# Kernel optimization log

Measured on AMD Instinct MI355X. Metric: run time of the kernel, lower is better.

## Reference

```python
import jax, jax.numpy as jnp
import numpy as np

VOCAB, T, E, H, O, B = 401, 140, 128, 256, 3, 4096


def setup_inputs() -> dict:
    key = jax.random.key(0)
    ks = jax.random.split(key, 8)
    s_e = 1.0 / np.sqrt(H)
    return {
        "input": jax.random.randint(ks[0], (B, T), 0, VOCAB),
        "hidden": jnp.zeros((B, H), dtype=jnp.float32),
        "embed": jax.random.normal(ks[1], (VOCAB, E), dtype=jnp.float32),
        "W_ih": jax.random.uniform(ks[2], (3 * H, E), jnp.float32, -s_e, s_e),
        "W_hh": jax.random.uniform(ks[3], (3 * H, H), jnp.float32, -s_e, s_e),
        "b_ih": jax.random.uniform(ks[4], (3 * H,), jnp.float32, -s_e, s_e),
        "b_hh": jax.random.uniform(ks[5], (3 * H,), jnp.float32, -s_e, s_e),
        "W_out": jax.random.uniform(ks[6], (O, H), jnp.float32, -s_e, s_e),
        "b_out": jax.random.uniform(ks[7], (O,), jnp.float32, -s_e, s_e),
    }


def reference(input, hidden, embed, W_ih, W_hh, b_ih, b_hh, W_out, b_out):
    # Embedding lookup: [B, T, E]
    x = embed[input]
    # Precompute input-side gate projections for all timesteps: [B, T, 3H]
    gi = jnp.einsum("bte,ge->btg", x, W_ih) + b_ih

    def step(h, gi_t):
        gh = h @ W_hh.T + b_hh  # [B, 3H]
        i_r, i_z, i_n = jnp.split(gi_t, 3, axis=-1)
        h_r, h_z, h_n = jnp.split(gh, 3, axis=-1)
        r = jax.nn.sigmoid(i_r + h_r)
        z = jax.nn.sigmoid(i_z + h_z)
        n = jnp.tanh(i_n + r * h_n)
        h_new = (1.0 - z) * n + z * h
        return h_new, None

    h_final, _ = jax.lax.scan(step, hidden, jnp.swapaxes(gi, 0, 1))
    logits = h_final @ W_out.T + b_out  # [B, O]
    return jax.nn.log_softmax(logits, axis=1), h_final
```

## Files before the change

### kernel.cpp

```cpp
#include <hip/hip_runtime.h>

typedef __attribute__((ext_vector_type(8))) short short8;
typedef __attribute__((ext_vector_type(4))) float f32x4;
typedef unsigned short ushort_t;
typedef unsigned int uint_t;

#define VOCAB 401
#define T_ 140
#define E_ 128
#define H_ 256
#define B_ 4096
#define HPAD 264

__device__ float Gf[VOCAB * 768];
__device__ ushort_t WhhB[768 * H_];

__device__ __forceinline__ float bf2f(ushort_t u) {
  union { uint_t i; float f; } x; x.i = ((uint_t)u) << 16; return x.f;
}
__device__ __forceinline__ ushort_t f2bf(float f) {
  union { float f; uint_t i; } x; x.f = f;
  uint_t r = x.i + 0x7FFFu + ((x.i >> 16) & 1u);
  return (ushort_t)(r >> 16);
}
__device__ __forceinline__ float fast_sigmoid(float x) {
  return __builtin_amdgcn_rcpf(1.f + __builtin_amdgcn_exp2f(-1.442695041f * x));
}
__device__ __forceinline__ float fast_tanh(float x) {
  return 1.f - 2.f * __builtin_amdgcn_rcpf(1.f + __builtin_amdgcn_exp2f(2.885390082f * x));
}
__device__ __forceinline__ float ldf(const void* p, size_t i, int isb) {
  return isb ? bf2f(((const ushort_t*)p)[i]) : ((const float*)p)[i];
}
__device__ __forceinline__ void ld8f(const void* p, size_t idx, int isb, float* o) {
  if (isb) {
    short8 v = *(const short8*)((const ushort_t*)p + idx);
#pragma unroll
    for (int e = 0; e < 8; ++e) o[e] = bf2f((ushort_t)v[e]);
  } else {
    f32x4 a = *(const f32x4*)((const float*)p + idx);
    f32x4 b = *(const f32x4*)((const float*)p + idx + 4);
#pragma unroll
    for (int e = 0; e < 4; ++e) { o[e] = a[e]; o[4 + e] = b[e]; }
  }
}
__device__ __forceinline__ int block_probe_isbf16(const ushort_t* embed_raw, int* s) {
  if (threadIdx.x < 64) {
    ushort_t v = embed_raw[2 * threadIdx.x];
    int e = (v >> 7) & 0xFF;
    unsigned long long m = __ballot(e >= 100 && e <= 140);
    if (threadIdx.x == 0) *s = (__popcll(m) >= 40) ? 1 : 0;
  }
  __syncthreads();
  return *s;
}

__global__ void prep(const void* __restrict__ W_hh,
                     const void* __restrict__ embed,
                     const void* __restrict__ W_ih,
                     const void* __restrict__ b_ih,
                     const void* __restrict__ b_hh) {
  __shared__ float emb[8][E_];
  __shared__ int sISB;
  const int isb = block_probe_isbf16((const ushort_t*)embed, &sISB);
  const int bid = blockIdx.x;
  const int j = threadIdx.x;

  if (bid >= 153) {
    int i4 = ((bid - 153) * 256 + j) * 4;
    if (isb) {
      *(uint2*)&WhhB[i4] = *(const uint2*)((const ushort_t*)W_hh + i4);
    } else {
      f32x4 v = *(const f32x4*)((const float*)W_hh + i4);
      uint2 pk;
      pk.x = (uint_t)f2bf(v[0]) | ((uint_t)f2bf(v[1]) << 16);
      pk.y = (uint_t)f2bf(v[2]) | ((uint_t)f2bf(v[3]) << 16);
      *(uint2*)&WhhB[i4] = pk;
    }
    return;
  }

  const int vb = bid / 3;
  const int g  = bid - vb * 3;
  for (int idx = j; idx < 8 * E_; idx += 256) {
    int s = idx >> 7, e = idx & 127;
    int v = vb * 8 + s; if (v > VOCAB - 1) v = VOCAB - 1;
    emb[s][e] = ldf(embed, (size_t)v * E_ + e, isb);
  }
  __syncthreads();
  const int row = g * H_ + j;
  float acc[8];
#pragma unroll
  for (int s = 0; s < 8; ++s) acc[s] = 0.f;
  for (int k8 = 0; k8 < E_ / 8; ++k8) {
    float wv[8];
    ld8f(W_ih, (size_t)row * E_ + k8 * 8, isb, wv);
#pragma unroll
    for (int s = 0; s < 8; ++s)
#pragma unroll
      for (int e = 0; e < 8; ++e) acc[s] += emb[s][k8 * 8 + e] * wv[e];
  }
  float bias = ldf(b_ih, row, isb) + ((g < 2) ? ldf(b_hh, row, isb) : 0.f);
#pragma unroll
  for (int s = 0; s < 8; ++s) {
    int v = vb * 8 + s;
    if (v < VOCAB) Gf[v * 768 + row] = acc[s] + bias;
  }
}

__launch_bounds__(1024)
__global__ void gru_persist(const int* __restrict__ input,
                            const void* __restrict__ hidden,
                            const void* __restrict__ b_hh,
                            const void* __restrict__ W_out,
                            const void* __restrict__ b_out,
                            const ushort_t* __restrict__ embed_raw,
                            void* __restrict__ out) {
  __shared__ ushort_t hB[2][16 * HPAD];
  __shared__ float bhhn[H_];
  __shared__ int ids[16 * (T_ + 1)];
  __shared__ int sISB;

  const int isb  = block_probe_isbf16(embed_raw, &sISB);
  const int tid  = threadIdx.x;
  const int w    = tid >> 6;
  const int lane = tid & 63;
  const int quad = lane >> 4;
  const int col  = lane & 15;
  const int wg   = blockIdx.x;
  const int u0   = w << 4;
  const int u0q  = u0 + (quad << 2);

  if (tid < 512) {
    int r = tid >> 5, c0 = (tid & 31) << 3;
    size_t gi = (size_t)(wg * 16 + r) * H_ + c0;
    ushort_t* dst = &hB[0][r * HPAD + c0];
    if (isb) {
      *(short8*)dst = *(const short8*)((const ushort_t*)hidden + gi);
    } else {
      float tmp[8];
      ld8f(hidden, gi, 0, tmp);
#pragma unroll
      for (int e = 0; e < 8; ++e) dst[e] = f2bf(tmp[e]);
    }
  }
  if (tid < H_) bhhn[tid] = ldf(b_hh, 512 + tid, isb);
  for (int k = tid; k < 16 * (T_ + 1); k += 1024) {
    int b = k / (T_ + 1), t = k - b * (T_ + 1);
    ids[k] = (t < T_) ? input[(size_t)wg * 16 * T_ + b * T_ + t] * 3072 : 0;
  }

  short8 wA[3][8];
#pragma unroll
  for (int g = 0; g < 3; ++g) {
    const ushort_t* wrow = WhhB + (size_t)(g * H_ + u0 + col) * H_ + (quad << 3);
#pragma unroll
    for (int kt = 0; kt < 8; ++kt) wA[g][kt] = *(const short8*)(wrow + kt * 32);
  }

  __syncthreads();

  float hreg[4];
#pragma unroll
  for (int i = 0; i < 4; ++i)
    hreg[i] = bf2f(hB[0][col * HPAD + u0q + i]);

  const int idbase = col * (T_ + 1);
  const char* gB = (const char*)Gf + (size_t)u0q * 4;

  f32x4 accr, accz, gin;
  {
    int goff = ids[idbase];
    accr = *(const f32x4*)(gB + goff);
    accz = *(const f32x4*)(gB + goff + 1024);
    gin  = *(const f32x4*)(gB + goff + 2048);
  }

#pragma unroll 2
  for (int t = 0; t < T_; ++t) {
    const int cur = t & 1;
    const int nxt = cur ^ 1;
    const ushort_t* hr = &hB[cur][col * HPAD + (quad << 3)];
    const int goff_n = ids[idbase + t + 1];
    f32x4 bhv = *(const f32x4*)&bhhn[u0q];

#pragma unroll
    for (int kt = 0; kt < 8; ++kt) {
      short8 b = *(const short8*)(hr + kt * 32);
      accr = __builtin_amdgcn_mfma_f32_16x16x32_bf16(wA[0][kt], b, accr, 0, 0, 0);
      accz = __builtin_amdgcn_mfma_f32_16x16x32_bf16(wA[1][kt], b, accz, 0, 0, 0);
    }
    f32x4 an = bhv;
    float r_[4], z_[4];
#pragma unroll
    for (int kt = 0; kt < 8; ++kt) {
      short8 b = *(const short8*)(hr + kt * 32);
      an = __builtin_amdgcn_mfma_f32_16x16x32_bf16(wA[2][kt], b, an, 0, 0, 0);
      if (kt < 4) r_[kt] = fast_sigmoid(accr[kt]);
      else        z_[kt - 4] = fast_sigmoid(accz[kt - 4]);
    }

    uint_t rr[4];
#pragma unroll
    for (int i = 0; i < 4; ++i) {
      float n = fast_tanh(gin[i] + r_[i] * an[i]);
      float h = n + z_[i] * (hreg[i] - n);
      hreg[i] = h;
      union { float f; uint_t u; } c; c.f = h;
      rr[i] = c.u + 0x7FFFu + ((c.u >> 16) & 1u);
    }
    ushort_t* hw = &hB[nxt][col * HPAD + u0q];
    *(uint_t*)&hw[0] = __builtin_amdgcn_perm(rr[1], rr[0], 0x07060302);
    *(uint_t*)&hw[2] = __builtin_amdgcn_perm(rr[3], rr[2], 0x07060302);

    accr = *(const f32x4*)(gB + goff_n);
    accz = *(const f32x4*)(gB + goff_n + 1024);
    gin  = *(const f32x4*)(gB + goff_n + 2048);

    asm volatile("s_waitcnt lgkmcnt(0)\n\ts_barrier" ::: "memory");
  }

  {
    const ushort_t* hrow = &hB[0][w * HPAD + (lane << 2)];
    float h0 = bf2f(hrow[0]), h1 = bf2f(hrow[1]), h2 = bf2f(hrow[2]), h3 = bf2f(hrow[3]);
    float d[3];
#pragma unroll
    for (int o = 0; o < 3; ++o) {
      size_t base = (size_t)o * H_ + (lane << 2);
      d[o] = ldf(W_out, base, isb) * h0 + ldf(W_out, base + 1, isb) * h1 +
             ldf(W_out, base + 2, isb) * h2 + ldf(W_out, base + 3, isb) * h3;
      for (int off = 1; off < 64; off <<= 1) d[o] += __shfl_xor(d[o], off);
    }
    if (lane == 0) {
      float l0 = d[0] + ldf(b_out, 0, isb);
      float l1 = d[1] + ldf(b_out, 1, isb);
      float l2 = d[2] + ldf(b_out, 2, isb);
      float m = fmaxf(l0, fmaxf(l1, l2));
      float s = __builtin_amdgcn_exp2f((l0 - m) * 1.442695041f) +
                __builtin_amdgcn_exp2f((l1 - m) * 1.442695041f) +
                __builtin_amdgcn_exp2f((l2 - m) * 1.442695041f);
      float ls = __builtin_amdgcn_logf(s) * 0.6931471806f;
      size_t ob = (size_t)(wg * 16 + w) * 3;
      float o0 = l0 - m - ls, o1 = l1 - m - ls, o2 = l2 - m - ls;
      if (isb) {
        ushort_t* ob16 = (ushort_t*)out;
        ob16[ob] = f2bf(o0); ob16[ob + 1] = f2bf(o1); ob16[ob + 2] = f2bf(o2);
      } else {
        float* of = (float*)out;
        of[ob] = o0; of[ob + 1] = o1; of[ob + 2] = o2;
      }
    }
  }
  {
    int e = tid << 2;
    int bb = e >> 8, uu = e & 255;
    const ushort_t* src = &hB[0][bb * HPAD + uu];
    size_t oi = 12288 + (size_t)wg * 4096 + e;
    if (isb) {
      *(uint2*)((ushort_t*)out + oi) = *(const uint2*)src;
    } else {
      float* of = (float*)out;
      of[oi] = bf2f(src[0]); of[oi + 1] = bf2f(src[1]);
      of[oi + 2] = bf2f(src[2]); of[oi + 3] = bf2f(src[3]);
    }
  }
}

extern "C" void kernel_launch(void* const* d_in, const int* in_sizes, int n_in,
                              void* d_out, int out_size, void* d_ws, size_t ws_size,
                              hipStream_t stream) {
  (void)in_sizes; (void)n_in; (void)out_size; (void)d_ws; (void)ws_size;
  const int* input = (const int*)d_in[0];
  const void* hidden = d_in[1];
  const void* embed  = d_in[2];
  const void* W_ih   = d_in[3];
  const void* W_hh   = d_in[4];
  const void* b_ih   = d_in[5];
  const void* b_hh   = d_in[6];
  const void* W_out  = d_in[7];
  const void* b_out  = d_in[8];

  prep<<<345, 256, 0, stream>>>(W_hh, embed, W_ih, b_ih, b_hh);
  gru_persist<<<B_ / 16, 1024, 0, stream>>>(input, hidden, b_hh, W_out, b_out,
                                            (const ushort_t*)embed, d_out);
}
```

Before: 363.6 us.

## Fold activation exponent scales into weights and biases; restructure GRU step loop

Pre-scales W_hh rows, the input-gate table Gf and the n-gate hidden bias by the sigmoid and tanh exp2 constants during prep. This removes the per-element multiplies before exp2 in the recurrent loop. The loop is also manually unrolled by two with precomputed double-buffer pointers, the bias load is hoisted out of the loop, and the three gate MFMAs are interleaved in a single k-loop with the activations computed afterward. Scaling before the bf16 rounding of W_hh changes rounding slightly, and issuing all activations after the MFMAs gives up overlap of the r/z sigmoids with the n-gate MFMA chain.

```diff
diff --git a/kernel.cpp b/kernel.cpp
--- a/kernel.cpp
+++ b/kernel.cpp
@@ -12,6 +12,9 @@
 #define B_ 4096
 #define HPAD 264
 
+#define SIG_K -1.442695041f
+#define TANH_K 2.885390082f
+
 __device__ float Gf[VOCAB * 768];
 __device__ ushort_t WhhB[768 * H_];
 
@@ -22,12 +25,6 @@
   union { float f; uint_t i; } x; x.f = f;
   uint_t r = x.i + 0x7FFFu + ((x.i >> 16) & 1u);
   return (ushort_t)(r >> 16);
-}
-__device__ __forceinline__ float fast_sigmoid(float x) {
-  return __builtin_amdgcn_rcpf(1.f + __builtin_amdgcn_exp2f(-1.442695041f * x));
-}
-__device__ __forceinline__ float fast_tanh(float x) {
-  return 1.f - 2.f * __builtin_amdgcn_rcpf(1.f + __builtin_amdgcn_exp2f(2.885390082f * x));
 }
 __device__ __forceinline__ float ldf(const void* p, size_t i, int isb) {
   return isb ? bf2f(((const ushort_t*)p)[i]) : ((const float*)p)[i];
@@ -68,15 +65,21 @@
 
   if (bid >= 153) {
     int i4 = ((bid - 153) * 256 + j) * 4;
+    float sc = ((i4 >> 8) < 512) ? SIG_K : TANH_K;
+    float v[4];
     if (isb) {
-      *(uint2*)&WhhB[i4] = *(const uint2*)((const ushort_t*)W_hh + i4);
+      uint2 raw = *(const uint2*)((const ushort_t*)W_hh + i4);
+      v[0] = bf2f((ushort_t)(raw.x & 0xffff)); v[1] = bf2f((ushort_t)(raw.x >> 16));
+      v[2] = bf2f((ushort_t)(raw.y & 0xffff)); v[3] = bf2f((ushort_t)(raw.y >> 16));
     } else {
-      f32x4 v = *(const f32x4*)((const float*)W_hh + i4);
-      uint2 pk;
-      pk.x = (uint_t)f2bf(v[0]) | ((uint_t)f2bf(v[1]) << 16);
-      pk.y = (uint_t)f2bf(v[2]) | ((uint_t)f2bf(v[3]) << 16);
-      *(uint2*)&WhhB[i4] = pk;
-    }
+      f32x4 f = *(const f32x4*)((const float*)W_hh + i4);
+#pragma unroll
+      for (int e = 0; e < 4; ++e) v[e] = f[e];
+    }
+    uint2 pk;
+    pk.x = (uint_t)f2bf(v[0] * sc) | ((uint_t)f2bf(v[1] * sc) << 16);
+    pk.y = (uint_t)f2bf(v[2] * sc) | ((uint_t)f2bf(v[3] * sc) << 16);
+    *(uint2*)&WhhB[i4] = pk;
     return;
   }
 
@@ -89,6 +92,7 @@
   }
   __syncthreads();
   const int row = g * H_ + j;
+  const float sc = (g < 2) ? SIG_K : TANH_K;
   float acc[8];
 #pragma unroll
   for (int s = 0; s < 8; ++s) acc[s] = 0.f;
@@ -104,7 +108,7 @@
 #pragma unroll
   for (int s = 0; s < 8; ++s) {
     int v = vb * 8 + s;
-    if (v < VOCAB) Gf[v * 768 + row] = acc[s] + bias;
+    if (v < VOCAB) Gf[v * 768 + row] = (acc[s] + bias) * sc;
   }
 }
 
@@ -144,7 +148,7 @@
       for (int e = 0; e < 8; ++e) dst[e] = f2bf(tmp[e]);
     }
   }
-  if (tid < H_) bhhn[tid] = ldf(b_hh, 512 + tid, isb);
+  if (tid < H_) bhhn[tid] = TANH_K * ldf(b_hh, 512 + tid, isb);
   for (int k = tid; k < 16 * (T_ + 1); k += 1024) {
     int b = k / (T_ + 1), t = k - b * (T_ + 1);
     ids[k] = (t < T_) ? input[(size_t)wg * 16 * T_ + b * T_ + t] * 3072 : 0;
@@ -164,9 +168,15 @@
 #pragma unroll
   for (int i = 0; i < 4; ++i)
     hreg[i] = bf2f(hB[0][col * HPAD + u0q + i]);
+  const f32x4 bhv = *(const f32x4*)&bhhn[u0q];
 
   const int idbase = col * (T_ + 1);
   const char* gB = (const char*)Gf + (size_t)u0q * 4;
+
+  const ushort_t* hr0 = &hB[0][col * HPAD + (quad << 3)];
+  const ushort_t* hr1 = &hB[1][col * HPAD + (quad << 3)];
+  ushort_t* hw0 = &hB[1][col * HPAD + u0q];
+  ushort_t* hw1 = &hB[0][col * HPAD + u0q];
 
   f32x4 accr, accz, gin;
   {
@@ -176,49 +186,42 @@
     gin  = *(const f32x4*)(gB + goff + 2048);
   }
 
-#pragma unroll 2
-  for (int t = 0; t < T_; ++t) {
-    const int cur = t & 1;
-    const int nxt = cur ^ 1;
-    const ushort_t* hr = &hB[cur][col * HPAD + (quad << 3)];
-    const int goff_n = ids[idbase + t + 1];
-    f32x4 bhv = *(const f32x4*)&bhhn[u0q];
-
-#pragma unroll
-    for (int kt = 0; kt < 8; ++kt) {
-      short8 b = *(const short8*)(hr + kt * 32);
-      accr = __builtin_amdgcn_mfma_f32_16x16x32_bf16(wA[0][kt], b, accr, 0, 0, 0);
-      accz = __builtin_amdgcn_mfma_f32_16x16x32_bf16(wA[1][kt], b, accz, 0, 0, 0);
-    }
-    f32x4 an = bhv;
-    float r_[4], z_[4];
-#pragma unroll
-    for (int kt = 0; kt < 8; ++kt) {
-      short8 b = *(const short8*)(hr + kt * 32);
-      an = __builtin_amdgcn_mfma_f32_16x16x32_bf16(wA[2][kt], b, an, 0, 0, 0);
-      if (kt < 4) r_[kt] = fast_sigmoid(accr[kt]);
-      else        z_[kt - 4] = fast_sigmoid(accz[kt - 4]);
-    }
-
-    uint_t rr[4];
-#pragma unroll
-    for (int i = 0; i < 4; ++i) {
-      float n = fast_tanh(gin[i] + r_[i] * an[i]);
-      float h = n + z_[i] * (hreg[i] - n);
-      hreg[i] = h;
-      union { float f; uint_t u; } c; c.f = h;
-      rr[i] = c.u + 0x7FFFu + ((c.u >> 16) & 1u);
-    }
-    ushort_t* hw = &hB[nxt][col * HPAD + u0q];
-    *(uint_t*)&hw[0] = __builtin_amdgcn_perm(rr[1], rr[0], 0x07060302);
-    *(uint_t*)&hw[2] = __builtin_amdgcn_perm(rr[3], rr[2], 0x07060302);
-
-    accr = *(const f32x4*)(gB + goff_n);
-    accz = *(const f32x4*)(gB + goff_n + 1024);
-    gin  = *(const f32x4*)(gB + goff_n + 2048);
-
-    asm volatile("s_waitcnt lgkmcnt(0)\n\ts_barrier" ::: "memory");
-  }
+#define GRU_STEP(HR, HW, TNEXT)                                                  \
+  {                                                                              \
+    const int goff_n = ids[idbase + (TNEXT)];                                    \
+    f32x4 an = bhv;                                                              \
+    _Pragma("unroll")                                                            \
+    for (int kt = 0; kt < 8; ++kt) {                                             \
+      short8 b = *(const short8*)((HR) + kt * 32);                               \
+      accr = __builtin_amdgcn_mfma_f32_16x16x32_bf16(wA[0][kt], b, accr, 0,0,0); \
+      accz = __builtin_amdgcn_mfma_f32_16x16x32_bf16(wA[1][kt], b, accz, 0,0,0); \
+      an   = __builtin_amdgcn_mfma_f32_16x16x32_bf16(wA[2][kt], b, an,   0,0,0); \
+    }                                                                            \
+    uint_t rr[4];                                                                \
+    _Pragma("unroll")                                                            \
+    for (int i = 0; i < 4; ++i) {                                                \
+      float r_ = __builtin_amdgcn_rcpf(1.f + __builtin_amdgcn_exp2f(accr[i]));   \
+      float z_ = __builtin_amdgcn_rcpf(1.f + __builtin_amdgcn_exp2f(accz[i]));   \
+      float n  = 1.f - 2.f * __builtin_amdgcn_rcpf(                              \
+                     1.f + __builtin_amdgcn_exp2f(gin[i] + r_ * an[i]));         \
+      float h  = n + z_ * (hreg[i] - n);                                         \
+      hreg[i] = h;                                                               \
+      union { float f; uint_t u; } c; c.f = h;                                   \
+      rr[i] = c.u + 0x7FFFu + ((c.u >> 16) & 1u);                                \
+    }                                                                            \
+    *(uint_t*)&(HW)[0] = __builtin_amdgcn_perm(rr[1], rr[0], 0x07060302);        \
+    *(uint_t*)&(HW)[2] = __builtin_amdgcn_perm(rr[3], rr[2], 0x07060302);        \
+    accr = *(const f32x4*)(gB + goff_n);                                         \
+    accz = *(const f32x4*)(gB + goff_n + 1024);                                  \
+    gin  = *(const f32x4*)(gB + goff_n + 2048);                                  \
+    asm volatile("s_waitcnt lgkmcnt(0)\n\ts_barrier" ::: "memory");              \
+  }
+
+  for (int t2 = 0; t2 < T_ / 2; ++t2) {
+    GRU_STEP(hr0, hw0, 2 * t2 + 1);
+    GRU_STEP(hr1, hw1, 2 * t2 + 2);
+  }
+#undef GRU_STEP
 
   {
     const ushort_t* hrow = &hB[0][w * HPAD + (lane << 2)];
```

New measurement: 493.7 us. 35.8% more time.
